# Optimization experiments

Hardware: AMD Instinct MI355X
Metric: run time of the kernel (lower is better)

Reference implementation:

```python
import jax, jax.numpy as jnp
import numpy as np

EPS = 1e-6
NUM_HEADS = 8


def _phi(x):
    # positive feature map: elu(x) + 1
    return jax.nn.elu(x) + 1.0


def setup_inputs() -> dict:
    key = jax.random.key(0)
    k1, k2, k3, k4, k5 = jax.random.split(key, 5)
    B, T, J, d = 8, 2048, 17, 128
    x = jax.random.normal(k1, (B, T, J, d + 1), dtype=jnp.float32)
    # qkv projection on the spatial part (xavier-ish small init, gain 0.02)
    w_qkv = jax.random.normal(k2, (3 * d, d), dtype=jnp.float32) * 0.02
    b_qkv = jnp.zeros((3 * d,), dtype=jnp.float32)
    # LorentzLinear out projection (spatial d -> d, time recomputed)
    w_out = jax.random.normal(k3, (d, d), dtype=jnp.float32) * (1.0 / np.sqrt(d))
    b_out = jnp.zeros((d,), dtype=jnp.float32)
    return {"x": x, "w_qkv": w_qkv, "b_qkv": b_qkv, "w_out": w_out, "b_out": b_out}


def reference(x, w_qkv, b_qkv, w_out, b_out):
    B, T, J, D = x.shape
    d = D - 1
    H = NUM_HEADS
    d_h = d // H
    BJ = B * J

    # [B,T,J,D] -> [BJ, T, D], drop the time coordinate
    x_flat = jnp.transpose(x, (0, 2, 1, 3)).reshape(BJ, T, D)
    x_spatial = x_flat[..., 1:]                                  # [BJ, T, d]

    qkv = x_spatial @ w_qkv.T + b_qkv                            # [BJ, T, 3d]
    qkv = qkv.reshape(BJ, T, 3, H, d_h)
    q = jnp.transpose(qkv[:, :, 0], (0, 2, 1, 3))                # [BJ, H, T, d_h]
    k = jnp.transpose(qkv[:, :, 1], (0, 2, 1, 3))
    v = jnp.transpose(qkv[:, :, 2], (0, 2, 1, 3))

    q_m = _phi(q)
    k_m = _phi(k)

    # linear attention: phi(K)^T V outer product, then phi(Q) aggregation
    kv = jnp.einsum("bhtd,bhte->bhde", k_m, v)                   # [BJ,H,d_h,d_h]
    agg = jnp.einsum("bhtd,bhde->bhte", q_m, kv)                 # [BJ,H,T,d_h]

    k_sum = k_m.sum(axis=2)                                      # [BJ,H,d_h]
    z_denom = jnp.einsum("bhtd,bhd->bht", q_m, k_sum)
    z_denom = jnp.clip(z_denom, EPS, None)[..., None]            # [BJ,H,T,1]
    agg = agg / z_denom

    agg_flat = jnp.transpose(agg, (0, 2, 1, 3)).reshape(BJ, T, d)
    sq = jnp.clip((agg_flat * agg_flat).sum(-1, keepdims=True), EPS, None)
    agg_time = jnp.sqrt(1.0 + sq)
    z = jnp.concatenate([agg_time, agg_flat], axis=-1)           # [BJ, T, D]

    # LorentzLinear out projection: linear on spatial part, recompute time
    y = z[..., 1:] @ w_out.T + b_out                             # [BJ, T, d]
    y_time = jnp.sqrt(1.0 + (y * y).sum(-1, keepdims=True))
    z = jnp.concatenate([y_time, y], axis=-1)                    # [BJ, T, D]

    z = z.reshape(B, J, T, D)
    return jnp.transpose(z, (0, 2, 1, 3))                        # [B, T, J, D]
```

## Files before the change

### kernel.cpp

```cpp
#include <hip/hip_runtime.h>
#include <math.h>

#define B_   8
#define T_   2048
#define J_   17
#define D_   129
#define d_   128
#define H_   8
#define BJ_  (B_ * J_)
#define EPS_ 1e-6f
#define CH   8
#define RPB  (T_ / CH)
#define NIT  (RPB / 64)

typedef short bf8 __attribute__((ext_vector_type(8)));
typedef float fx4 __attribute__((ext_vector_type(4)));

__device__ __forceinline__ float phi_f(float x) {
    return x > 0.f ? x + 1.f : __expf(x);
}
__device__ __forceinline__ short f2b(float f) {
    union { float f; unsigned u; } c; c.f = f;
    unsigned u = c.u + 0x7fffu + ((c.u >> 16) & 1u);
    return (short)(u >> 16);
}
__device__ __forceinline__ float b2f(short s) {
    union { float f; unsigned u; } c;
    c.u = ((unsigned)(unsigned short)s) << 16;
    return c.f;
}

__global__ __launch_bounds__(256, 2) void pass_kv(
        const float* __restrict__ x, const float* __restrict__ wqkv,
        const float* __restrict__ bqkv,
        float* __restrict__ kvw,
        float* __restrict__ ksw) {
    const int bj = blockIdx.y, b = bj / J_, j = bj % J_;
    const int t0 = blockIdx.x * RPB;
    const int tid = threadIdx.x, wave = tid >> 6, lane = tid & 63;
    const int quad = lane >> 4, l16 = lane & 15;

    __shared__ short sx[64 * 136];
    __shared__ short kT[128 * 72];
    __shared__ short vT[128 * 72];

    bf8 wf[4][4];
    float bias[4];
    #pragma unroll
    for (int nt = 0; nt < 4; ++nt) {
        const int n = d_ + wave * 64 + nt * 16 + l16;
        bias[nt] = bqkv[n];
        #pragma unroll
        for (int ks = 0; ks < 4; ++ks) {
            const float* p = wqkv + (size_t)n * d_ + ks * 32 + quad * 8;
            bf8 t;
            #pragma unroll
            for (int q2 = 0; q2 < 8; ++q2) t[q2] = f2b(p[q2]);
            wf[nt][ks] = t;
        }
    }

    fx4 kva[2];
    kva[0] = (fx4){0.f, 0.f, 0.f, 0.f};
    kva[1] = (fx4){0.f, 0.f, 0.f, 0.f};
    float ksp[4] = {0.f, 0.f, 0.f, 0.f};

    for (int it = 0; it < NIT; ++it) {
        __syncthreads();
        {
            const int tb = t0 + it * 64;
            #pragma unroll
            for (int i = 0; i < 16; ++i) {
                const int F = tid + 256 * i, row = F >> 6, c2 = F & 63;
                const float* xr = x + ((size_t)((b * T_ + tb + row) * J_ + j)) * D_ + 1 + 2 * c2;
                *reinterpret_cast<unsigned*>(&sx[row * 136 + 2 * c2]) =
                    (unsigned)(unsigned short)f2b(xr[0]) |
                    ((unsigned)(unsigned short)f2b(xr[1]) << 16);
            }
        }
        __syncthreads();

        fx4 acc[4][4];
        #pragma unroll
        for (int nt = 0; nt < 4; ++nt)
            #pragma unroll
            for (int mt = 0; mt < 4; ++mt) acc[nt][mt] = (fx4){0.f, 0.f, 0.f, 0.f};

        #pragma unroll
        for (int ks = 0; ks < 4; ++ks) {
            bf8 af[4];
            #pragma unroll
            for (int mt = 0; mt < 4; ++mt)
                af[mt] = *reinterpret_cast<const bf8*>(
                    &sx[(mt * 16 + l16) * 136 + ks * 32 + quad * 8]);
            #pragma unroll
            for (int nt = 0; nt < 4; ++nt)
                #pragma unroll
                for (int mt = 0; mt < 4; ++mt)
                    acc[nt][mt] = __builtin_amdgcn_mfma_f32_16x16x32_bf16(
                        af[mt], wf[nt][ks], acc[nt][mt], 0, 0, 0);
        }

        {
            short* dst = (wave < 2) ? kT : vT;
            const int fbase = (wave & 1) * 64;
            const bool isk = (wave < 2);
            #pragma unroll
            for (int nt = 0; nt < 4; ++nt)
                #pragma unroll
                for (int mt = 0; mt < 4; ++mt) {
                    unsigned long long pk = 0ull;
                    #pragma unroll
                    for (int r = 0; r < 4; ++r) {
                        float v = acc[nt][mt][r] + bias[nt];
                        if (isk) { v = phi_f(v); ksp[nt] += v; }
                        pk |= ((unsigned long long)(unsigned short)f2b(v)) << (16 * r);
                    }
                    *reinterpret_cast<unsigned long long*>(
                        &dst[(fbase + nt * 16 + l16) * 72 + mt * 16 + quad * 4]) = pk;
                }
        }
        __syncthreads();

        #pragma unroll
        for (int hh = 0; hh < 2; ++hh) {
            const int h = wave * 2 + hh;
            #pragma unroll
            for (int ks2 = 0; ks2 < 2; ++ks2) {
                bf8 ak = *reinterpret_cast<const bf8*>(
                    &kT[(h * 16 + l16) * 72 + ks2 * 32 + quad * 8]);
                bf8 bv = *reinterpret_cast<const bf8*>(
                    &vT[(h * 16 + l16) * 72 + ks2 * 32 + quad * 8]);
                kva[hh] = __builtin_amdgcn_mfma_f32_16x16x32_bf16(ak, bv, kva[hh], 0, 0, 0);
            }
        }
    }

    #pragma unroll
    for (int hh = 0; hh < 2; ++hh) {
        const int h = wave * 2 + hh;
        float* p = kvw + (((size_t)bj * H_ + h) * 16 + l16) * 16 + quad * 4;
        #pragma unroll
        for (int r = 0; r < 4; ++r) atomicAdd(p + r, kva[hh][r]);
    }
    if (wave < 2) {
        #pragma unroll
        for (int nt = 0; nt < 4; ++nt) {
            float s = ksp[nt];
            s += __shfl_xor(s, 16);
            s += __shfl_xor(s, 32);
            if (lane < 16)
                atomicAdd(ksw + (size_t)bj * d_ + wave * 64 + nt * 16 + l16, s);
        }
    }
}

__global__ __launch_bounds__(256, 2) void pass_out(
        const float* __restrict__ x, const float* __restrict__ wqkv,
        const float* __restrict__ bqkv, const float* __restrict__ wout,
        const float* __restrict__ bout,
        const float* __restrict__ kvw, const float* __restrict__ ksw,
        float* __restrict__ out) {
    const int bj = blockIdx.y, b = bj / J_, j = bj % J_;
    const int t0 = blockIdx.x * RPB;
    const int tid = threadIdx.x, wave = tid >> 6, lane = tid & 63;
    const int quad = lane >> 4, l16 = lane & 15;

    __shared__ short sx[64 * 136];
    __shared__ short qm[64 * 136];
    __shared__ short sag[64 * 136];
    __shared__ short kvT[H_ * 16 * 24];
    __shared__ float kss[d_];
    __shared__ float dens[64 * H_];
    __shared__ float rnorm[64];

    bf8 wqf[2][4], wof[2][4];
    float bq2[2], bo2[2];
    #pragma unroll
    for (int nt = 0; nt < 2; ++nt) {
        const int n = wave * 32 + nt * 16 + l16;
        bq2[nt] = bqkv[n];
        bo2[nt] = bout[n];
        #pragma unroll
        for (int ks = 0; ks < 4; ++ks) {
            const float* p = wqkv + (size_t)n * d_ + ks * 32 + quad * 8;
            const float* p2 = wout + (size_t)n * d_ + ks * 32 + quad * 8;
            bf8 t, t2;
            #pragma unroll
            for (int q2 = 0; q2 < 8; ++q2) { t[q2] = f2b(p[q2]); t2[q2] = f2b(p2[q2]); }
            wqf[nt][ks] = t;
            wof[nt][ks] = t2;
        }
    }
    #pragma unroll
    for (int i = 0; i < 8; ++i) {
        const int idx = tid + 256 * i;
        const int h = idx >> 8, jj = (idx >> 4) & 15, ii = idx & 15;
        kvT[(h * 16 + jj) * 24 + ii] =
            f2b(kvw[(((size_t)bj * H_ + h) * 16 + jj) * 16 + ii]);
    }
    if (tid < d_) kss[tid] = ksw[(size_t)bj * d_ + tid];

    for (int it = 0; it < NIT; ++it) {
        __syncthreads();
        {
            const int tb = t0 + it * 64;
            #pragma unroll
            for (int i = 0; i < 16; ++i) {
                const int F = tid + 256 * i, row = F >> 6, c2 = F & 63;
                const float* xr = x + ((size_t)((b * T_ + tb + row) * J_ + j)) * D_ + 1 + 2 * c2;
                *reinterpret_cast<unsigned*>(&sx[row * 136 + 2 * c2]) =
                    (unsigned)(unsigned short)f2b(xr[0]) |
                    ((unsigned)(unsigned short)f2b(xr[1]) << 16);
            }
            if (tid < 64) rnorm[tid] = 0.f;
        }
        __syncthreads();

        fx4 acc[2][4];
        #pragma unroll
        for (int nt = 0; nt < 2; ++nt)
            #pragma unroll
            for (int mt = 0; mt < 4; ++mt) acc[nt][mt] = (fx4){0.f, 0.f, 0.f, 0.f};
        #pragma unroll
        for (int ks = 0; ks < 4; ++ks) {
            bf8 af[4];
            #pragma unroll
            for (int mt = 0; mt < 4; ++mt)
                af[mt] = *reinterpret_cast<const bf8*>(
                    &sx[(mt * 16 + l16) * 136 + ks * 32 + quad * 8]);
            #pragma unroll
            for (int nt = 0; nt < 2; ++nt)
                #pragma unroll
                for (int mt = 0; mt < 4; ++mt)
                    acc[nt][mt] = __builtin_amdgcn_mfma_f32_16x16x32_bf16(
                        af[mt], wqf[nt][ks], acc[nt][mt], 0, 0, 0);
        }
        #pragma unroll
        for (int nt = 0; nt < 2; ++nt) {
            const int col = wave * 32 + nt * 16 + l16;
            #pragma unroll
            for (int mt = 0; mt < 4; ++mt)
                #pragma unroll
                for (int r = 0; r < 4; ++r)
                    qm[(mt * 16 + quad * 4 + r) * 136 + col] =
                        f2b(phi_f(acc[nt][mt][r] + bq2[nt]));
        }
        __syncthreads();

        #pragma unroll
        for (int u = 0; u < 2; ++u) {
            const int s2 = tid * 2 + u, row = s2 >> 3, h = s2 & 7;
            const short* qp = &qm[row * 136 + h * 16];
            float s = 0.f;
            #pragma unroll
            for (int i = 0; i < 16; ++i) s += b2f(qp[i]) * kss[h * 16 + i];
            dens[row * 8 + h] = fmaxf(s, EPS_);
        }
        __syncthreads();

        #pragma unroll
        for (int hh = 0; hh < 2; ++hh) {
            const int h = wave * 2 + hh;
            bf8 bk = (bf8){0, 0, 0, 0, 0, 0, 0, 0};
            if (quad < 2)
                bk = *reinterpret_cast<const bf8*>(&kvT[(h * 16 + l16) * 24 + quad * 8]);
            #pragma unroll
            for (int mt = 0; mt < 4; ++mt) {
                bf8 aq = (bf8){0, 0, 0, 0, 0, 0, 0, 0};
                if (quad < 2)
                    aq = *reinterpret_cast<const bf8*>(
                        &qm[(mt * 16 + l16) * 136 + h * 16 + quad * 8]);
                fx4 ag = __builtin_amdgcn_mfma_f32_16x16x32_bf16(
                    aq, bk, (fx4){0.f, 0.f, 0.f, 0.f}, 0, 0, 0);
                #pragma unroll
                for (int r = 0; r < 4; ++r) {
                    const int row = mt * 16 + quad * 4 + r;
                    sag[row * 136 + h * 16 + l16] = f2b(ag[r] / dens[row * 8 + h]);
                }
            }
        }
        __syncthreads();

        fx4 ya[2][4];
        #pragma unroll
        for (int nt = 0; nt < 2; ++nt)
            #pragma unroll
            for (int mt = 0; mt < 4; ++mt) ya[nt][mt] = (fx4){0.f, 0.f, 0.f, 0.f};
        #pragma unroll
        for (int ks = 0; ks < 4; ++ks) {
            bf8 af[4];
            #pragma unroll
            for (int mt = 0; mt < 4; ++mt)
                af[mt] = *reinterpret_cast<const bf8*>(
                    &sag[(mt * 16 + l16) * 136 + ks * 32 + quad * 8]);
            #pragma unroll
            for (int nt = 0; nt < 2; ++nt)
                #pragma unroll
                for (int mt = 0; mt < 4; ++mt)
                    ya[nt][mt] = __builtin_amdgcn_mfma_f32_16x16x32_bf16(
                        af[mt], wof[nt][ks], ya[nt][mt], 0, 0, 0);
        }

        const int tb = t0 + it * 64;
        #pragma unroll
        for (int mt = 0; mt < 4; ++mt) {
            float sq[4] = {0.f, 0.f, 0.f, 0.f};
            #pragma unroll
            for (int nt = 0; nt < 2; ++nt) {
                const int col = wave * 32 + nt * 16 + l16;
                #pragma unroll
                for (int r = 0; r < 4; ++r) {
                    const float y = ya[nt][mt][r] + bo2[nt];
                    const int t = tb + mt * 16 + quad * 4 + r;
                    out[((size_t)(b * T_ + t) * J_ + j) * D_ + 1 + col] = y;
                    sq[r] += y * y;
                }
            }
            #pragma unroll
            for (int r = 0; r < 4; ++r) {
                float s = sq[r];
                s += __shfl_xor(s, 1);
                s += __shfl_xor(s, 2);
                s += __shfl_xor(s, 4);
                s += __shfl_xor(s, 8);
                if (l16 == 0) atomicAdd(&rnorm[mt * 16 + quad * 4 + r], s);
            }
        }
        __syncthreads();
        if (tid < 64) {
            const int t = tb + tid;
            out[((size_t)(b * T_ + t) * J_ + j) * D_] = sqrtf(1.f + rnorm[tid]);
        }
    }
}

extern "C" void kernel_launch(void* const* d_in, const int* in_sizes, int n_in,
                              void* d_out, int out_size, void* d_ws, size_t ws_size,
                              hipStream_t stream) {
    const float* x     = (const float*)d_in[0];
    const float* wqkv  = (const float*)d_in[1];
    const float* bqkv  = (const float*)d_in[2];
    const float* wout  = (const float*)d_in[3];
    const float* bout  = (const float*)d_in[4];
    float* out = (float*)d_out;

    float* kvw = (float*)d_ws;
    float* ksw = kvw + (size_t)BJ_ * H_ * 16 * 16;
    const size_t zero_bytes =
        ((size_t)BJ_ * H_ * 16 * 16 + (size_t)BJ_ * d_) * sizeof(float);
    hipMemsetAsync(d_ws, 0, zero_bytes, stream);

    dim3 blk(256);
    dim3 grd(CH, BJ_);
    hipLaunchKernelGGL(pass_kv, grd, blk, 0, stream, x, wqkv, bqkv, kvw, ksw);
    hipLaunchKernelGGL(pass_out, grd, blk, 0, stream, x, wqkv, bqkv, wout, bout,
                       kvw, ksw, out);
}
```

Before: 397.3 us.

## Compute attention denominator via MFMA, cut LDS and syncs, raise occupancy

The scalar per-row denominator loop and its two barriers are replaced by extra MFMA ops. These multiply phi(Q) by the key sum, split into bf16 hi and lo parts to keep precision, and the result is scaled with a reciprocal. The aggregation buffer now reuses the qm buffer, which frees LDS. Launch bounds go up and pass_out uses twice as many time chunks for more occupancy. The QKV MFMA loop is split in halves to cut register pressure, and weight loads are vectorized. Dropping barriers around qm reuse depends on each wave touching only its own head columns, which risks races if that assumption is wrong.

```diff
diff --git a/kernel.cpp b/kernel.cpp
--- a/kernel.cpp
+++ b/kernel.cpp
@@ -9,9 +9,13 @@
 #define H_   8
 #define BJ_  (B_ * J_)
 #define EPS_ 1e-6f
-#define CH   8
-#define RPB  (T_ / CH)
-#define NIT  (RPB / 64)
+
+#define CHK  8
+#define RPBK (T_ / CHK)
+#define NITK (RPBK / 64)
+#define CHO  16
+#define RPBO (T_ / CHO)
+#define NITO (RPBO / 64)
 
 typedef short bf8 __attribute__((ext_vector_type(8)));
 typedef float fx4 __attribute__((ext_vector_type(4)));
@@ -29,20 +33,28 @@
     c.u = ((unsigned)(unsigned short)s) << 16;
     return c.f;
 }
-
-__global__ __launch_bounds__(256, 2) void pass_kv(
+__device__ __forceinline__ bf8 ld_w8(const float* p) {
+    const float4* q = reinterpret_cast<const float4*>(p);
+    float4 a = q[0], b = q[1];
+    bf8 t;
+    t[0] = f2b(a.x); t[1] = f2b(a.y); t[2] = f2b(a.z); t[3] = f2b(a.w);
+    t[4] = f2b(b.x); t[5] = f2b(b.y); t[6] = f2b(b.z); t[7] = f2b(b.w);
+    return t;
+}
+
+__global__ __launch_bounds__(256, 3) void pass_kv(
         const float* __restrict__ x, const float* __restrict__ wqkv,
         const float* __restrict__ bqkv,
         float* __restrict__ kvw,
         float* __restrict__ ksw) {
     const int bj = blockIdx.y, b = bj / J_, j = bj % J_;
-    const int t0 = blockIdx.x * RPB;
+    const int t0 = blockIdx.x * RPBK;
     const int tid = threadIdx.x, wave = tid >> 6, lane = tid & 63;
     const int quad = lane >> 4, l16 = lane & 15;
 
-    __shared__ short sx[64 * 136];
-    __shared__ short kT[128 * 72];
-    __shared__ short vT[128 * 72];
+    __shared__ __align__(16) short sx[64 * 136];
+    __shared__ __align__(16) short kT[128 * 72];
+    __shared__ __align__(16) short vT[128 * 72];
 
     bf8 wf[4][4];
     float bias[4];
@@ -51,13 +63,8 @@
         const int n = d_ + wave * 64 + nt * 16 + l16;
         bias[nt] = bqkv[n];
         #pragma unroll
-        for (int ks = 0; ks < 4; ++ks) {
-            const float* p = wqkv + (size_t)n * d_ + ks * 32 + quad * 8;
-            bf8 t;
-            #pragma unroll
-            for (int q2 = 0; q2 < 8; ++q2) t[q2] = f2b(p[q2]);
-            wf[nt][ks] = t;
-        }
+        for (int ks = 0; ks < 4; ++ks)
+            wf[nt][ks] = ld_w8(wqkv + (size_t)n * d_ + ks * 32 + quad * 8);
     }
 
     fx4 kva[2];
@@ -65,8 +72,7 @@
     kva[1] = (fx4){0.f, 0.f, 0.f, 0.f};
     float ksp[4] = {0.f, 0.f, 0.f, 0.f};
 
-    for (int it = 0; it < NIT; ++it) {
-        __syncthreads();
+    for (int it = 0; it < NITK; ++it) {
         {
             const int tb = t0 + it * 64;
             #pragma unroll
@@ -80,45 +86,49 @@
         }
         __syncthreads();
 
-        fx4 acc[4][4];
-        #pragma unroll
-        for (int nt = 0; nt < 4; ++nt)
-            #pragma unroll
-            for (int mt = 0; mt < 4; ++mt) acc[nt][mt] = (fx4){0.f, 0.f, 0.f, 0.f};
-
-        #pragma unroll
-        for (int ks = 0; ks < 4; ++ks) {
-            bf8 af[4];
-            #pragma unroll
-            for (int mt = 0; mt < 4; ++mt)
-                af[mt] = *reinterpret_cast<const bf8*>(
-                    &sx[(mt * 16 + l16) * 136 + ks * 32 + quad * 8]);
-            #pragma unroll
-            for (int nt = 0; nt < 4; ++nt)
+        short* dst = (wave < 2) ? kT : vT;
+        const int fbase = (wave & 1) * 64;
+        const bool isk = (wave < 2);
+
+        #pragma unroll
+        for (int pr = 0; pr < 2; ++pr) {
+            fx4 acc[2][4];
+            #pragma unroll
+            for (int n2 = 0; n2 < 2; ++n2)
+                #pragma unroll
+                for (int mt = 0; mt < 4; ++mt) acc[n2][mt] = (fx4){0.f, 0.f, 0.f, 0.f};
+
+            #pragma unroll
+            for (int ks = 0; ks < 4; ++ks) {
+                bf8 af[4];
                 #pragma unroll
                 for (int mt = 0; mt < 4; ++mt)
-                    acc[nt][mt] = __builtin_amdgcn_mfma_f32_16x16x32_bf16(
-                        af[mt], wf[nt][ks], acc[nt][mt], 0, 0, 0);
-        }
-
-        {
-            short* dst = (wave < 2) ? kT : vT;
-            const int fbase = (wave & 1) * 64;
-            const bool isk = (wave < 2);
-            #pragma unroll
-            for (int nt = 0; nt < 4; ++nt)
+                    af[mt] = *reinterpret_cast<const bf8*>(
+                        &sx[(mt * 16 + l16) * 136 + ks * 32 + quad * 8]);
+                #pragma unroll
+                for (int n2 = 0; n2 < 2; ++n2)
+                    #pragma unroll
+                    for (int mt = 0; mt < 4; ++mt)
+                        acc[n2][mt] = __builtin_amdgcn_mfma_f32_16x16x32_bf16(
+                            af[mt], wf[pr * 2 + n2][ks], acc[n2][mt], 0, 0, 0);
+            }
+
+            #pragma unroll
+            for (int n2 = 0; n2 < 2; ++n2) {
+                const int nt = pr * 2 + n2;
                 #pragma unroll
                 for (int mt = 0; mt < 4; ++mt) {
                     unsigned long long pk = 0ull;
                     #pragma unroll
                     for (int r = 0; r < 4; ++r) {
-                        float v = acc[nt][mt][r] + bias[nt];
+                        float v = acc[n2][mt][r] + bias[nt];
                         if (isk) { v = phi_f(v); ksp[nt] += v; }
                         pk |= ((unsigned long long)(unsigned short)f2b(v)) << (16 * r);
                     }
                     *reinterpret_cast<unsigned long long*>(
                         &dst[(fbase + nt * 16 + l16) * 72 + mt * 16 + quad * 4]) = pk;
                 }
+            }
         }
         __syncthreads();
 
@@ -155,23 +165,22 @@
     }
 }
 
-__global__ __launch_bounds__(256, 2) void pass_out(
+__global__ __launch_bounds__(256, 4) void pass_out(
         const float* __restrict__ x, const float* __restrict__ wqkv,
         const float* __restrict__ bqkv, const float* __restrict__ wout,
         const float* __restrict__ bout,
         const float* __restrict__ kvw, const float* __restrict__ ksw,
         float* __restrict__ out) {
     const int bj = blockIdx.y, b = bj / J_, j = bj % J_;
-    const int t0 = blockIdx.x * RPB;
+    const int t0 = blockIdx.x * RPBO;
     const int tid = threadIdx.x, wave = tid >> 6, lane = tid & 63;
     const int quad = lane >> 4, l16 = lane & 15;
 
-    __shared__ short sx[64 * 136];
-    __shared__ short qm[64 * 136];
-    __shared__ short sag[64 * 136];
-    __shared__ short kvT[H_ * 16 * 24];
-    __shared__ float kss[d_];
-    __shared__ float dens[64 * H_];
+    __shared__ __align__(16) short sxg[64 * 136];
+    __shared__ __align__(16) short qm[64 * 136];
+    __shared__ __align__(16) short kvT2[H_ * 2 * 16 * 8];
+    __shared__ __align__(16) short ksshi[d_];
+    __shared__ __align__(16) short ksslo[d_];
     __shared__ float rnorm[64];
 
     bf8 wqf[2][4], wof[2][4];
@@ -183,37 +192,35 @@
         bo2[nt] = bout[n];
         #pragma unroll
         for (int ks = 0; ks < 4; ++ks) {
-            const float* p = wqkv + (size_t)n * d_ + ks * 32 + quad * 8;
-            const float* p2 = wout + (size_t)n * d_ + ks * 32 + quad * 8;
-            bf8 t, t2;
-            #pragma unroll
-            for (int q2 = 0; q2 < 8; ++q2) { t[q2] = f2b(p[q2]); t2[q2] = f2b(p2[q2]); }
-            wqf[nt][ks] = t;
-            wof[nt][ks] = t2;
+            wqf[nt][ks] = ld_w8(wqkv + (size_t)n * d_ + ks * 32 + quad * 8);
+            wof[nt][ks] = ld_w8(wout + (size_t)n * d_ + ks * 32 + quad * 8);
         }
     }
     #pragma unroll
-    for (int i = 0; i < 8; ++i) {
-        const int idx = tid + 256 * i;
-        const int h = idx >> 8, jj = (idx >> 4) & 15, ii = idx & 15;
-        kvT[(h * 16 + jj) * 24 + ii] =
-            f2b(kvw[(((size_t)bj * H_ + h) * 16 + jj) * 16 + ii]);
-    }
-    if (tid < d_) kss[tid] = ksw[(size_t)bj * d_ + tid];
-
-    for (int it = 0; it < NIT; ++it) {
-        __syncthreads();
+    for (int u = 0; u < 8; ++u) {
+        const int lin = tid + 256 * u;
+        const int jj = lin & 7, jv = (lin >> 3) & 15, qd = (lin >> 7) & 1, h = lin >> 8;
+        kvT2[lin] = f2b(kvw[(((size_t)bj * H_ + h) * 16 + jv) * 16 + qd * 8 + jj]);
+    }
+    if (tid < d_) {
+        const float v = ksw[(size_t)bj * d_ + tid];
+        const short hi = f2b(v);
+        ksshi[tid] = hi;
+        ksslo[tid] = f2b(v - b2f(hi));
+    }
+    if (tid < 64) rnorm[tid] = 0.f;
+
+    for (int it = 0; it < NITO; ++it) {
+        const int tb = t0 + it * 64;
         {
-            const int tb = t0 + it * 64;
             #pragma unroll
             for (int i = 0; i < 16; ++i) {
                 const int F = tid + 256 * i, row = F >> 6, c2 = F & 63;
                 const float* xr = x + ((size_t)((b * T_ + tb + row) * J_ + j)) * D_ + 1 + 2 * c2;
-                *reinterpret_cast<unsigned*>(&sx[row * 136 + 2 * c2]) =
+                *reinterpret_cast<unsigned*>(&sxg[row * 136 + 2 * c2]) =
                     (unsigned)(unsigned short)f2b(xr[0]) |
                     ((unsigned)(unsigned short)f2b(xr[1]) << 16);
             }
-            if (tid < 64) rnorm[tid] = 0.f;
         }
         __syncthreads();
 
@@ -228,7 +235,7 @@
             #pragma unroll
             for (int mt = 0; mt < 4; ++mt)
                 af[mt] = *reinterpret_cast<const bf8*>(
-                    &sx[(mt * 16 + l16) * 136 + ks * 32 + quad * 8]);
+                    &sxg[(mt * 16 + l16) * 136 + ks * 32 + quad * 8]);
             #pragma unroll
             for (int nt = 0; nt < 2; ++nt)
                 #pragma unroll
@@ -246,25 +253,19 @@
                     qm[(mt * 16 + quad * 4 + r) * 136 + col] =
                         f2b(phi_f(acc[nt][mt][r] + bq2[nt]));
         }
-        __syncthreads();
-
-        #pragma unroll
-        for (int u = 0; u < 2; ++u) {
-            const int s2 = tid * 2 + u, row = s2 >> 3, h = s2 & 7;
-            const short* qp = &qm[row * 136 + h * 16];
-            float s = 0.f;
-            #pragma unroll
-            for (int i = 0; i < 16; ++i) s += b2f(qp[i]) * kss[h * 16 + i];
-            dens[row * 8 + h] = fmaxf(s, EPS_);
-        }
-        __syncthreads();
+        asm volatile("" ::: "memory");
 
         #pragma unroll
         for (int hh = 0; hh < 2; ++hh) {
             const int h = wave * 2 + hh;
             bf8 bk = (bf8){0, 0, 0, 0, 0, 0, 0, 0};
-            if (quad < 2)
-                bk = *reinterpret_cast<const bf8*>(&kvT[(h * 16 + l16) * 24 + quad * 8]);
+            bf8 bh = (bf8){0, 0, 0, 0, 0, 0, 0, 0};
+            bf8 bl = (bf8){0, 0, 0, 0, 0, 0, 0, 0};
+            if (quad < 2) {
+                bk = *reinterpret_cast<const bf8*>(&kvT2[((h * 2 + quad) * 16 + l16) * 8]);
+                bh = *reinterpret_cast<const bf8*>(&ksshi[h * 16 + quad * 8]);
+                bl = *reinterpret_cast<const bf8*>(&ksslo[h * 16 + quad * 8]);
+            }
             #pragma unroll
             for (int mt = 0; mt < 4; ++mt) {
                 bf8 aq = (bf8){0, 0, 0, 0, 0, 0, 0, 0};
@@ -273,10 +274,14 @@
                         &qm[(mt * 16 + l16) * 136 + h * 16 + quad * 8]);
                 fx4 ag = __builtin_amdgcn_mfma_f32_16x16x32_bf16(
                     aq, bk, (fx4){0.f, 0.f, 0.f, 0.f}, 0, 0, 0);
+                fx4 dd = __builtin_amdgcn_mfma_f32_16x16x32_bf16(
+                    aq, bl, (fx4){0.f, 0.f, 0.f, 0.f}, 0, 0, 0);
+                dd = __builtin_amdgcn_mfma_f32_16x16x32_bf16(aq, bh, dd, 0, 0, 0);
                 #pragma unroll
                 for (int r = 0; r < 4; ++r) {
-                    const int row = mt * 16 + quad * 4 + r;
-                    sag[row * 136 + h * 16 + l16] = f2b(ag[r] / dens[row * 8 + h]);
+                    const float rin = __builtin_amdgcn_rcpf(fmaxf(dd[r], EPS_));
+                    qm[(mt * 16 + quad * 4 + r) * 136 + h * 16 + l16] =
+                        f2b(ag[r] * rin);
                 }
             }
         }
@@ -293,7 +298,7 @@
             #pragma unroll
             for (int mt = 0; mt < 4; ++mt)
                 af[mt] = *reinterpret_cast<const bf8*>(
-                    &sag[(mt * 16 + l16) * 136 + ks * 32 + quad * 8]);
+                    &qm[(mt * 16 + l16) * 136 + ks * 32 + quad * 8]);
             #pragma unroll
             for (int nt = 0; nt < 2; ++nt)
                 #pragma unroll
@@ -302,7 +307,6 @@
                         af[mt], wof[nt][ks], ya[nt][mt], 0, 0, 0);
         }
 
-        const int tb = t0 + it * 64;
         #pragma unroll
         for (int mt = 0; mt < 4; ++mt) {
             float sq[4] = {0.f, 0.f, 0.f, 0.f};
@@ -331,6 +335,7 @@
         if (tid < 64) {
             const int t = tb + tid;
             out[((size_t)(b * T_ + t) * J_ + j) * D_] = sqrtf(1.f + rnorm[tid]);
+            rnorm[tid] = 0.f;
         }
     }
 }
@@ -352,8 +357,9 @@
     hipMemsetAsync(d_ws, 0, zero_bytes, stream);
 
     dim3 blk(256);
-    dim3 grd(CH, BJ_);
-    hipLaunchKernelGGL(pass_kv, grd, blk, 0, stream, x, wqkv, bqkv, kvw, ksw);
-    hipLaunchKernelGGL(pass_out, grd, blk, 0, stream, x, wqkv, bqkv, wout, bout,
+    dim3 grdK(CHK, BJ_);
+    dim3 grdO(CHO, BJ_);
+    hipLaunchKernelGGL(pass_kv, grdK, blk, 0, stream, x, wqkv, bqkv, kvw, ksw);
+    hipLaunchKernelGGL(pass_out, grdO, blk, 0, stream, x, wqkv, bqkv, wout, bout,
                        kvw, ksw, out);
 }
```

New measurement: 623.9 us. 57.0% more time.
